# Performance work log

Hardware: AMD Instinct MI355X
Metric: run time of the kernel (lower is better)

The kernel has to match this reference:

```python
import jax, jax.numpy as jnp
import numpy as np

N_NODES = 100_000
N_EDGES = 1_600_000
N_GRAPHS = 1_000
VOCAB = 65
D_IN = 128
D_HID = 128


def setup_inputs() -> dict:
    key = jax.random.key(0)
    ks = jax.random.split(key, 12)
    x = jax.random.randint(ks[0], (N_NODES,), 0, VOCAB)
    edge_index = jax.random.randint(ks[1], (2, N_EDGES), 0, N_NODES)
    batch = jnp.sort(jax.random.randint(ks[2], (N_NODES,), 0, N_GRAPHS))

    def lin(k, fan_in, fan_out):
        bound = 1.0 / np.sqrt(fan_in)
        kw, kb = jax.random.split(k)
        W = jax.random.uniform(kw, (fan_in, fan_out), jnp.float32, -bound, bound)
        b = jax.random.uniform(kb, (fan_out,), jnp.float32, -bound, bound)
        return W, b

    emb = jax.random.normal(ks[3], (VOCAB, D_IN), jnp.float32)
    W1, b1 = lin(ks[4], D_IN, D_HID)
    W2, b2 = lin(ks[5], D_HID, D_HID)
    W3, b3 = lin(ks[6], D_HID, D_HID)
    Wf, bf = lin(ks[7], D_HID, 1)
    return {"x": x, "edge_index": edge_index, "batch": batch, "emb": emb,
            "W1": W1, "b1": b1, "W2": W2, "b2": b2, "W3": W3, "b3": b3,
            "Wf": Wf, "bf": bf}


def gcn_conv(h, W, b, src, dst, n):
    # PyG GCNConv: add self-loops, symmetric normalization D^-1/2 A_hat D^-1/2,
    # transform then aggregate messages at dst.
    h = h @ W                                             # [N, H]
    deg = jnp.zeros((n,), h.dtype).at[dst].add(1.0) + 1.0  # self-loop adds 1
    dinv = jax.lax.rsqrt(deg)                             # [N]
    coef = dinv[src] * dinv[dst]                          # [E]
    agg = jax.ops.segment_sum(h[src] * coef[:, None], dst, num_segments=n)
    return agg + h * (dinv * dinv)[:, None] + b           # self-loop term + bias


def reference(x, edge_index, batch, emb, W1, b1, W2, b2, W3, b3, Wf, bf):
    # Embedding with max_norm=1: renormalize looked-up rows to norm <= 1.
    e = emb[x]                                            # [N, D_IN]
    nrm = jnp.linalg.norm(e, axis=-1, keepdims=True)
    e = e * jnp.minimum(1.0, 1.0 / jnp.maximum(nrm, 1e-7))

    src, dst = edge_index[0], edge_index[1]
    h = jax.nn.relu(gcn_conv(e, W1, b1, src, dst, N_NODES))
    h = jax.nn.relu(gcn_conv(h, W2, b2, src, dst, N_NODES))
    h = jax.nn.relu(gcn_conv(h, W3, b3, src, dst, N_NODES))

    g = jax.ops.segment_max(h, batch, num_segments=N_GRAPHS)  # [G, H]
    return (g @ Wf + bf).ravel()                               # [G]
```

## Files before the change

kernel.cpp:

```cpp
#include <hip/hip_runtime.h>
#include <hip/hip_bf16.h>

#define N_NODES  100000
#define N_EDGES  1600000
#define N_GRAPHS 1000
#define D        128
#define CAP      64
#define NBKT     256
#define N_BUCKETS ((N_NODES + NBKT - 1) / NBKT)
#define HWGS     256
#define EPW      ((N_EDGES + HWGS - 1) / HWGS)
#define BNDB     ((N_NODES + 255) / 256)

typedef __attribute__((ext_vector_type(8))) short bf16x8;
typedef __attribute__((ext_vector_type(4))) float f32x4;

__device__ inline f32x4 mfma16(bf16x8 a, bf16x8 b, f32x4 c) {
    return __builtin_amdgcn_mfma_f32_16x16x32_bf16(a, b, c, 0, 0, 0);
}

__device__ inline unsigned short f2bf(float f) {
    unsigned u = __float_as_uint(f);
    unsigned r = u + 0x7fffu + ((u >> 16) & 1u);
    return (unsigned short)(r >> 16);
}

__global__ __launch_bounds__(256) void k_hist(const int* __restrict__ dst,
                                              int* __restrict__ bcnt,
                                              int* __restrict__ wgoff,
                                              const float* __restrict__ W1,
                                              const float* __restrict__ W2,
                                              const float* __restrict__ W3,
                                              short* __restrict__ frag,
                                              const int* __restrict__ batch,
                                              int* __restrict__ gstart,
                                              int* __restrict__ gend) {
    int w = blockIdx.x, t = threadIdx.x;
    if (w >= HWGS + 3) {
        int gid = (w - HWGS - 3) * 256 + t;
        if (gid < N_NODES) {
            int b = batch[gid];
            if (gid == 0 || batch[gid - 1] != b) gstart[b] = gid;
            if (gid == N_NODES - 1 || batch[gid + 1] != b) gend[b] = gid + 1;
        }
        return;
    }
    if (w >= HWGS) {
        int L = w - HWGS;
        const float* W = (L == 0) ? W1 : (L == 1) ? W2 : W3;
        short* fh = frag + (size_t)L * 16384;
        #pragma unroll
        for (int f = 0; f < 8; f++) {
            int id = t + f * 256;
            int lane = id & 63, kb = (id >> 6) & 3, nt = id >> 8;
            int k0 = kb * 32 + (lane >> 4) * 8;
            int n  = nt * 16 + (lane & 15);
            bf16x8 vh;
            #pragma unroll
            for (int j = 0; j < 8; j++)
                vh[j] = (short)f2bf(W[(k0 + j) * 128 + n]);
            *(bf16x8*)&fh[id * 8] = vh;
        }
        return;
    }
    __shared__ int hist[N_BUCKETS];
    for (int b = t; b < N_BUCKETS; b += 256) hist[b] = 0;
    __syncthreads();
    int e0 = w * EPW, e1 = min(e0 + EPW, N_EDGES);
    for (int i = e0 + t; i < e1; i += 256)
        atomicAdd(&hist[dst[i] >> 8], 1);
    __syncthreads();
    for (int b = t; b < N_BUCKETS; b += 256) {
        int h = hist[b];
        wgoff[w * N_BUCKETS + b] = h ? atomicAdd(&bcnt[b], h) : 0;
    }
}

__global__ __launch_bounds__(256) void k_scat(const int* __restrict__ src,
                                              const int* __restrict__ dst,
                                              const int* __restrict__ bcnt,
                                              const int* __restrict__ wgoff,
                                              int* __restrict__ ep) {
    __shared__ int sc[2][512];
    __shared__ int boff_s[N_BUCKETS];
    __shared__ int cnt[N_BUCKETS];
    int t = threadIdx.x, w = blockIdx.x;
    for (int i = t; i < 512; i += 256) sc[0][i] = (i < N_BUCKETS) ? bcnt[i] : 0;
    for (int b = t; b < N_BUCKETS; b += 256) cnt[b] = 0;
    __syncthreads();
    int pp = 0;
    for (int off = 1; off < 512; off <<= 1) {
        for (int i = t; i < 512; i += 256) {
            int v = sc[pp][i];
            if (i >= off) v += sc[pp][i - off];
            sc[1 - pp][i] = v;
        }
        __syncthreads();
        pp ^= 1;
    }
    for (int i = t; i < N_BUCKETS; i += 256) boff_s[i] = i ? sc[pp][i - 1] : 0;
    __syncthreads();
    int e0 = w * EPW, e1 = min(e0 + EPW, N_EDGES);
    for (int i = e0 + t; i < e1; i += 256) {
        int d = dst[i], b = d >> 8;
        int r = atomicAdd(&cnt[b], 1);
        ep[boff_s[b] + wgoff[w * N_BUCKETS + b] + r] = (src[i] << 8) | (d & 255);
    }
}

__global__ __launch_bounds__(256) void k_ell(const int* __restrict__ ep,
                                             const int* __restrict__ bcnt,
                                             int* __restrict__ ell,
                                             int* __restrict__ fill) {
    __shared__ int red[256];
    __shared__ int cnt_s[NBKT];
    __shared__ int ell_s[NBKT * CAP];
    int t = threadIdx.x, b = blockIdx.x;
    int partial = 0;
    for (int i = t; i < b; i += 256) partial += bcnt[i];
    red[t] = partial;
    for (int i = t; i < NBKT; i += 256) cnt_s[i] = 0;
    __syncthreads();
    for (int off = 128; off; off >>= 1) {
        if (t < off) red[t] += red[t + off];
        __syncthreads();
    }
    int e0 = red[0];
    int e1 = e0 + bcnt[b];
    int nb0 = b * NBKT;
    int nn = min(NBKT, N_NODES - nb0);
    for (int i = e0 + t; i < e1; i += 256) {
        int e = ep[i];
        int ln = e & 255;
        int r = atomicAdd(&cnt_s[ln], 1);
        if (r < CAP) ell_s[ln * CAP + r] = (int)((unsigned)e >> 8);
    }
    __syncthreads();
    for (int i = t; i < nn * CAP; i += 256)
        ell[(size_t)nb0 * CAP + i] = ell_s[i];
    if (t < nn) fill[nb0 + t] = cnt_s[t];
}

__device__ inline void gemm_body(const short* Bf,
                                 const bf16x8* a0, const bf16x8* a1,
                                 f32x4 acc[2][8], int lane) {
    #pragma unroll
    for (int kb = 0; kb < 4; kb++)
        #pragma unroll
        for (int nt = 0; nt < 8; nt++) {
            bf16x8 b = *(const bf16x8*)&Bf[((nt * 4 + kb) * 64 + lane) * 8];
            acc[0][nt] = mfma16(a0[kb], b, acc[0][nt]);
            acc[1][nt] = mfma16(a1[kb], b, acc[1][nt]);
        }
}

__device__ inline void gemm_epilogue(f32x4 acc[2][8], const int* fill,
                                     unsigned short* Cb, size_t r0,
                                     int quad, int col) {
    #pragma unroll
    for (int r = 0; r < 2; r++) {
        size_t row = r0 + r * 16 + quad * 4;
        #pragma unroll
        for (int g = 0; g < 4; g++) {
            float dv = (row + g < N_NODES)
                         ? 1.0f / sqrtf((float)fill[row + g] + 1.0f) : 0.f;
            #pragma unroll
            for (int nt = 0; nt < 8; nt++)
                Cb[(row + g) * D + nt * 16 + col] = f2bf(acc[r][nt][g] * dv);
        }
    }
}

__global__ __launch_bounds__(256) void k_gemm1e(const int* __restrict__ x,
                                                const float* __restrict__ emb,
                                                const short* __restrict__ frag,
                                                const int* __restrict__ fill,
                                                unsigned short* __restrict__ Cb) {
    __shared__ short Bfrag[16384];
    int t = threadIdx.x;
    {
        const int4* g4 = (const int4*)frag;
        int4* l4 = (int4*)Bfrag;
        #pragma unroll
        for (int i = 0; i < 8; i++) l4[t + i * 256] = g4[t + i * 256];
    }
    int w = t >> 6, lane = t & 63;
    int quad = lane >> 4, col = lane & 15;
    size_t r0 = (size_t)blockIdx.x * 128 + w * 32;

    bf16x8 a0[4], a1[4];
    {
        size_t ra = r0 + col, rb = r0 + 16 + col;
        int xa = (ra < N_NODES) ? x[ra] : 0;
        int xb = (rb < N_NODES) ? x[rb] : 0;
        float va[32], vb[32];
        float ssa = 0.f, ssb = 0.f;
        #pragma unroll
        for (int kb = 0; kb < 4; kb++) {
            float4 pa0 = *(const float4*)&emb[(size_t)xa * D + kb * 32 + quad * 8];
            float4 pa1 = *(const float4*)&emb[(size_t)xa * D + kb * 32 + quad * 8 + 4];
            float4 pb0 = *(const float4*)&emb[(size_t)xb * D + kb * 32 + quad * 8];
            float4 pb1 = *(const float4*)&emb[(size_t)xb * D + kb * 32 + quad * 8 + 4];
            va[kb*8+0]=pa0.x; va[kb*8+1]=pa0.y; va[kb*8+2]=pa0.z; va[kb*8+3]=pa0.w;
            va[kb*8+4]=pa1.x; va[kb*8+5]=pa1.y; va[kb*8+6]=pa1.z; va[kb*8+7]=pa1.w;
            vb[kb*8+0]=pb0.x; vb[kb*8+1]=pb0.y; vb[kb*8+2]=pb0.z; vb[kb*8+3]=pb0.w;
            vb[kb*8+4]=pb1.x; vb[kb*8+5]=pb1.y; vb[kb*8+6]=pb1.z; vb[kb*8+7]=pb1.w;
            #pragma unroll
            for (int j = 0; j < 8; j++) { ssa += va[kb*8+j]*va[kb*8+j];
                                          ssb += vb[kb*8+j]*vb[kb*8+j]; }
        }
        ssa += __shfl_xor(ssa, 16); ssa += __shfl_xor(ssa, 32);
        ssb += __shfl_xor(ssb, 16); ssb += __shfl_xor(ssb, 32);
        float sca = fminf(1.0f, 1.0f / fmaxf(sqrtf(ssa), 1e-7f));
        float scb = fminf(1.0f, 1.0f / fmaxf(sqrtf(ssb), 1e-7f));
        #pragma unroll
        for (int kb = 0; kb < 4; kb++) {
            bf16x8 fa, fb;
            #pragma unroll
            for (int j = 0; j < 8; j++) {
                fa[j] = (short)f2bf(va[kb*8+j] * sca);
                fb[j] = (short)f2bf(vb[kb*8+j] * scb);
            }
            a0[kb] = fa; a1[kb] = fb;
        }
    }
    f32x4 acc[2][8];
    #pragma unroll
    for (int r = 0; r < 2; r++)
        #pragma unroll
        for (int n = 0; n < 8; n++) acc[r][n] = (f32x4){0.f, 0.f, 0.f, 0.f};
    __syncthreads();
    gemm_body(Bfrag, a0, a1, acc, lane);
    gemm_epilogue(acc, fill, Cb, r0, quad, col);
}

__global__ __launch_bounds__(256) void k_gemm(const unsigned short* __restrict__ A,
                                              const short* __restrict__ frag,
                                              const int* __restrict__ fill,
                                              unsigned short* __restrict__ Cb) {
    __shared__ short Bfrag[16384];
    int t = threadIdx.x;
    {
        const int4* g4 = (const int4*)frag;
        int4* l4 = (int4*)Bfrag;
        #pragma unroll
        for (int i = 0; i < 8; i++) l4[t + i * 256] = g4[t + i * 256];
    }
    __syncthreads();
    int w = t >> 6, lane = t & 63;
    int quad = lane >> 4, col = lane & 15;
    size_t r0 = (size_t)blockIdx.x * 128 + w * 32;
    bf16x8 a0[4], a1[4];
    #pragma unroll
    for (int kb = 0; kb < 4; kb++) {
        a0[kb] = *(const bf16x8*)&A[(r0 + col)      * D + kb * 32 + quad * 8];
        a1[kb] = *(const bf16x8*)&A[(r0 + 16 + col) * D + kb * 32 + quad * 8];
    }
    f32x4 acc[2][8];
    #pragma unroll
    for (int r = 0; r < 2; r++)
        #pragma unroll
        for (int n = 0; n < 8; n++) acc[r][n] = (f32x4){0.f, 0.f, 0.f, 0.f};
    gemm_body(Bfrag, a0, a1, acc, lane);
    gemm_epilogue(acc, fill, Cb, r0, quad, col);
}

__device__ inline void acc8(float* acc, int4 r) {
    unsigned u0 = (unsigned)r.x, u1 = (unsigned)r.y,
             u2 = (unsigned)r.z, u3 = (unsigned)r.w;
    acc[0] += __uint_as_float(u0 << 16);
    acc[1] += __uint_as_float(u0 & 0xffff0000u);
    acc[2] += __uint_as_float(u1 << 16);
    acc[3] += __uint_as_float(u1 & 0xffff0000u);
    acc[4] += __uint_as_float(u2 << 16);
    acc[5] += __uint_as_float(u2 & 0xffff0000u);
    acc[6] += __uint_as_float(u3 << 16);
    acc[7] += __uint_as_float(u3 & 0xffff0000u);
}

#define LOADGRP(R, S, IT)                                                    \
    {                                                                        \
        _Pragma("unroll")                                                    \
        for (int k = 0; k < 4; k++) {                                        \
            int s = __shfl((S), (IT) * 16 + k * 4 + quad);                   \
            R[k] = *(const int4*)&hw2[((unsigned)s << 7) + cOff];            \
        }                                                                    \
    }
#define ACCGRP(A, R)                                                         \
    {                                                                        \
        _Pragma("unroll")                                                    \
        for (int k = 0; k < 4; k++) acc8((A), R[k]);                         \
    }

__global__ __launch_bounds__(256) void k_agg(const unsigned short* __restrict__ hw2,
                                             unsigned short* __restrict__ hout,
                                             const int* __restrict__ fill,
                                             const int* __restrict__ ell,
                                             const float* __restrict__ bias) {
    int w = threadIdx.x >> 6, lane = threadIdx.x & 63;
    int na = blockIdx.x * 8 + w * 2;
    int nb = na + 1;
    if (na >= N_NODES) return;
    int quad = lane >> 4;
    int l16  = lane & 15;
    unsigned cOff = (unsigned)(l16 << 3);

    int fa = __builtin_amdgcn_readfirstlane(fill[na]);
    int fb = __builtin_amdgcn_readfirstlane(fill[nb]);
    int ca = min(fa, CAP), cb = min(fb, CAP);
    int sa = (lane < ca) ? ell[na * CAP + lane] : N_NODES;
    int sb = (lane < cb) ? ell[nb * CAP + lane] : N_NODES;
    int ia = (ca + 15) >> 4; ia += (ia == 0);
    int ib = (cb + 15) >> 4; ib += (ib == 0);

    float accA[8], accB[8];
    #pragma unroll
    for (int c = 0; c < 8; c++) { accA[c] = 0.f; accB[c] = 0.f; }

    int4 A0[4], A1[4], B0[4], B1[4];
    LOADGRP(A0, sa, 0);
    LOADGRP(B0, sb, 0);
    if (1 < ia) LOADGRP(A1, sa, 1);
    ACCGRP(accA, A0);
    if (1 < ib) LOADGRP(B1, sb, 1);
    ACCGRP(accB, B0);
    if (ia > 1 || ib > 1) {
        if (2 < ia) LOADGRP(A0, sa, 2);
        if (1 < ia) ACCGRP(accA, A1);
        if (2 < ib) LOADGRP(B0, sb, 2);
        if (1 < ib) ACCGRP(accB, B1);
        if (ia > 2 || ib > 2) {
            if (3 < ia) LOADGRP(A1, sa, 3);
            if (2 < ia) ACCGRP(accA, A0);
            if (3 < ib) LOADGRP(B1, sb, 3);
            if (2 < ib) ACCGRP(accB, B0);
            if (3 < ia) ACCGRP(accA, A1);
            if (3 < ib) ACCGRP(accB, B1);
        }
    }

    #pragma unroll
    for (int c = 0; c < 8; c++) {
        accA[c] += __shfl_xor(accA[c], 16);
        accA[c] += __shfl_xor(accA[c], 32);
        accB[c] += __shfl_xor(accB[c], 16);
        accB[c] += __shfl_xor(accB[c], 32);
    }
    if (quad < 2) {
        int   n   = quad ? nb : na;
        int   fr  = quad ? fb : fa;
        float* acc = quad ? accB : accA;
        int4 sr = *(const int4*)&hw2[((unsigned)n << 7) + cOff];
        acc8(acc, sr);
        float di = 1.0f / sqrtf((float)fr + 1.0f);
        float4 bA = *(const float4*)&bias[l16 * 8];
        float4 bB = *(const float4*)&bias[l16 * 8 + 4];
        float o[8];
        o[0] = fmaxf(acc[0] * di + bA.x, 0.f);
        o[1] = fmaxf(acc[1] * di + bA.y, 0.f);
        o[2] = fmaxf(acc[2] * di + bA.z, 0.f);
        o[3] = fmaxf(acc[3] * di + bA.w, 0.f);
        o[4] = fmaxf(acc[4] * di + bB.x, 0.f);
        o[5] = fmaxf(acc[5] * di + bB.y, 0.f);
        o[6] = fmaxf(acc[6] * di + bB.z, 0.f);
        o[7] = fmaxf(acc[7] * di + bB.w, 0.f);
        int4 pk;
        pk.x = (int)((unsigned)f2bf(o[0]) | ((unsigned)f2bf(o[1]) << 16));
        pk.y = (int)((unsigned)f2bf(o[2]) | ((unsigned)f2bf(o[3]) << 16));
        pk.z = (int)((unsigned)f2bf(o[4]) | ((unsigned)f2bf(o[5]) << 16));
        pk.w = (int)((unsigned)f2bf(o[6]) | ((unsigned)f2bf(o[7]) << 16));
        *(int4*)&hout[((unsigned)n << 7) + cOff] = pk;
    }
}

__global__ __launch_bounds__(256) void k_pool(const unsigned short* __restrict__ h,
                                              const int* __restrict__ gstart,
                                              const int* __restrict__ gend,
                                              const float* __restrict__ Wf,
                                              const float* __restrict__ bf,
                                              float* __restrict__ out) {
    __shared__ float2 sm[4][64];
    int g = blockIdx.x;
    int w = threadIdx.x >> 6, lane = threadIdx.x & 63;
    int s = gstart[g], e = gend[g];
    float2 m = make_float2(-3.402823466e38f, -3.402823466e38f);
    for (int i = s + w; i < e; i += 4) {
        unsigned u = ((const unsigned*)(h + (size_t)i * D))[lane];
        m.x = fmaxf(m.x, __uint_as_float(u << 16));
        m.y = fmaxf(m.y, __uint_as_float(u & 0xffff0000u));
    }
    sm[w][lane] = m;
    __syncthreads();
    if (w == 0) {
        float2 a = sm[0][lane], b2 = sm[1][lane], c = sm[2][lane], d = sm[3][lane];
        m.x = fmaxf(fmaxf(a.x, b2.x), fmaxf(c.x, d.x));
        m.y = fmaxf(fmaxf(a.y, b2.y), fmaxf(c.y, d.y));
        float2 wf = ((const float2*)Wf)[lane];
        float val = m.x * wf.x + m.y * wf.y;
        #pragma unroll
        for (int off = 32; off; off >>= 1) val += __shfl_xor(val, off);
        if (lane == 0) out[g] = val + bf[0];
    }
}

extern "C" void kernel_launch(void* const* d_in, const int* in_sizes, int n_in,
                              void* d_out, int out_size, void* d_ws, size_t ws_size,
                              hipStream_t stream) {
    const int*   x    = (const int*)d_in[0];
    const int*   ei   = (const int*)d_in[1];
    const int*   batch= (const int*)d_in[2];
    const float* emb  = (const float*)d_in[3];
    const float* W1   = (const float*)d_in[4];
    const float* b1   = (const float*)d_in[5];
    const float* W2   = (const float*)d_in[6];
    const float* b2   = (const float*)d_in[7];
    const float* W3   = (const float*)d_in[8];
    const float* b3   = (const float*)d_in[9];
    const float* Wf   = (const float*)d_in[10];
    const float* bf   = (const float*)d_in[11];
    float* out = (float*)d_out;

    const int* src = ei;
    const int* dst = ei + N_EDGES;

    char* p = (char*)d_ws;
    unsigned short* hAb  = (unsigned short*)p; p += (size_t)(N_NODES + 128) * D * 2;
    unsigned short* hwb  = (unsigned short*)p; p += (size_t)(N_NODES + 128) * D * 2;
    int*            ep   = (int*)hwb;
    int*   fill     = (int*)p;              p += (size_t)N_NODES * 4;
    int*   gbounds  = (int*)p;              p += (size_t)2 * N_GRAPHS * 4;
    int*   ell      = (int*)p;              p += (size_t)N_NODES * CAP * 4;
    int*   wgoff    = (int*)p;              p += (size_t)HWGS * N_BUCKETS * 4;
    int*   bcnt     = (int*)p;              p += (size_t)(N_BUCKETS + 4) * 4;
    short* wfrag    = (short*)p;            p += (size_t)3 * 16384 * 2;
    (void)p;
    int* gstart = gbounds;
    int* gend   = gbounds + N_GRAPHS;

    hipMemsetAsync(bcnt, 0, (size_t)N_BUCKETS * 4, stream);

    const int GB = (N_NODES + 127) / 128;
    const int AB = N_NODES / 8;

    k_hist<<<HWGS + 3 + BNDB, 256, 0, stream>>>(dst, bcnt, wgoff, W1, W2, W3,
                                                wfrag, batch, gstart, gend);
    k_scat<<<HWGS, 256, 0, stream>>>(src, dst, bcnt, wgoff, ep);
    k_ell <<<N_BUCKETS, 256, 0, stream>>>(ep, bcnt, ell, fill);

    k_gemm1e<<<GB, 256, 0, stream>>>(x, emb, wfrag, fill, hwb);
    k_agg   <<<AB, 256, 0, stream>>>(hwb, hAb, fill, ell, b1);
    k_gemm<<<GB, 256, 0, stream>>>(hAb, wfrag + 16384, fill, hwb);
    k_agg <<<AB, 256, 0, stream>>>(hwb, hAb, fill, ell, b2);
    k_gemm<<<GB, 256, 0, stream>>>(hAb, wfrag + 32768, fill, hwb);
    k_agg <<<AB, 256, 0, stream>>>(hwb, hAb, fill, ell, b3);

    k_pool<<<N_GRAPHS, 256, 0, stream>>>(hAb, gstart, gend, Wf, bf, out);
}
```

Measured before the change: 374.5 us.

## Replace histogram-prefix edge bucketing with fixed-slot per-workgroup scatter

Drops the separate histogram kernel, the global bucket-count memset and the prefix scan. Each workgroup now scatters its edges straight into a fixed 64-slot region per (bucket, workgroup) and records per-segment counts. The ELL builder walks these padded segments instead of a compacted edge array. This removes a launch and a global synchronisation point, but the ELL kernel reads more sparsely populated memory, and edges are silently dropped if any workgroup gives a bucket more than 64 edges.

```diff
diff --git a/kernel.cpp b/kernel.cpp
--- a/kernel.cpp
+++ b/kernel.cpp
@@ -11,6 +11,7 @@
 #define HWGS     256
 #define EPW      ((N_EDGES + HWGS - 1) / HWGS)
 #define BNDB     ((N_NODES + 255) / 256)
+#define SLOT     64
 
 typedef __attribute__((ext_vector_type(8))) short bf16x8;
 typedef __attribute__((ext_vector_type(4))) float f32x4;
@@ -25,9 +26,10 @@
     return (unsigned short)(r >> 16);
 }
 
-__global__ __launch_bounds__(256) void k_hist(const int* __restrict__ dst,
-                                              int* __restrict__ bcnt,
-                                              int* __restrict__ wgoff,
+__global__ __launch_bounds__(256) void k_scat(const int* __restrict__ src,
+                                              const int* __restrict__ dst,
+                                              int* __restrict__ ep2,
+                                              int* __restrict__ cnt,
                                               const float* __restrict__ W1,
                                               const float* __restrict__ W2,
                                               const float* __restrict__ W3,
@@ -63,79 +65,46 @@
         }
         return;
     }
-    __shared__ int hist[N_BUCKETS];
-    for (int b = t; b < N_BUCKETS; b += 256) hist[b] = 0;
-    __syncthreads();
-    int e0 = w * EPW, e1 = min(e0 + EPW, N_EDGES);
-    for (int i = e0 + t; i < e1; i += 256)
-        atomicAdd(&hist[dst[i] >> 8], 1);
-    __syncthreads();
-    for (int b = t; b < N_BUCKETS; b += 256) {
-        int h = hist[b];
-        wgoff[w * N_BUCKETS + b] = h ? atomicAdd(&bcnt[b], h) : 0;
-    }
-}
-
-__global__ __launch_bounds__(256) void k_scat(const int* __restrict__ src,
-                                              const int* __restrict__ dst,
-                                              const int* __restrict__ bcnt,
-                                              const int* __restrict__ wgoff,
-                                              int* __restrict__ ep) {
-    __shared__ int sc[2][512];
-    __shared__ int boff_s[N_BUCKETS];
-    __shared__ int cnt[N_BUCKETS];
-    int t = threadIdx.x, w = blockIdx.x;
-    for (int i = t; i < 512; i += 256) sc[0][i] = (i < N_BUCKETS) ? bcnt[i] : 0;
-    for (int b = t; b < N_BUCKETS; b += 256) cnt[b] = 0;
-    __syncthreads();
-    int pp = 0;
-    for (int off = 1; off < 512; off <<= 1) {
-        for (int i = t; i < 512; i += 256) {
-            int v = sc[pp][i];
-            if (i >= off) v += sc[pp][i - off];
-            sc[1 - pp][i] = v;
-        }
-        __syncthreads();
-        pp ^= 1;
-    }
-    for (int i = t; i < N_BUCKETS; i += 256) boff_s[i] = i ? sc[pp][i - 1] : 0;
+    __shared__ int cnt_l[N_BUCKETS];
+    for (int b = t; b < N_BUCKETS; b += 256) cnt_l[b] = 0;
     __syncthreads();
     int e0 = w * EPW, e1 = min(e0 + EPW, N_EDGES);
     for (int i = e0 + t; i < e1; i += 256) {
         int d = dst[i], b = d >> 8;
-        int r = atomicAdd(&cnt[b], 1);
-        ep[boff_s[b] + wgoff[w * N_BUCKETS + b] + r] = (src[i] << 8) | (d & 255);
-    }
-}
-
-__global__ __launch_bounds__(256) void k_ell(const int* __restrict__ ep,
-                                             const int* __restrict__ bcnt,
+        int r = atomicAdd(&cnt_l[b], 1);
+        if (r < SLOT)
+            ep2[(size_t)b * (HWGS * SLOT) + w * SLOT + r] =
+                (src[i] << 8) | (d & 255);
+    }
+    __syncthreads();
+    for (int b = t; b < N_BUCKETS; b += 256)
+        cnt[w * N_BUCKETS + b] = cnt_l[b];
+}
+
+__global__ __launch_bounds__(256) void k_ell(const int* __restrict__ ep2,
+                                             const int* __restrict__ cnt,
                                              int* __restrict__ ell,
                                              int* __restrict__ fill) {
-    __shared__ int red[256];
+    __shared__ int cseg[HWGS];
     __shared__ int cnt_s[NBKT];
     __shared__ int ell_s[NBKT * CAP];
     int t = threadIdx.x, b = blockIdx.x;
-    int partial = 0;
-    for (int i = t; i < b; i += 256) partial += bcnt[i];
-    red[t] = partial;
+    cseg[t] = min(cnt[t * N_BUCKETS + b], SLOT);
     for (int i = t; i < NBKT; i += 256) cnt_s[i] = 0;
     __syncthreads();
-    for (int off = 128; off; off >>= 1) {
-        if (t < off) red[t] += red[t + off];
-        __syncthreads();
-    }
-    int e0 = red[0];
-    int e1 = e0 + bcnt[b];
+    size_t base = (size_t)b * (HWGS * SLOT);
+    for (int i = t; i < HWGS * SLOT; i += 256) {
+        int w = i >> 6, slot = i & (SLOT - 1);
+        if (slot < cseg[w]) {
+            int e = ep2[base + i];
+            int ln = e & 255;
+            int r = atomicAdd(&cnt_s[ln], 1);
+            if (r < CAP) ell_s[ln * CAP + r] = (int)((unsigned)e >> 8);
+        }
+    }
+    __syncthreads();
     int nb0 = b * NBKT;
     int nn = min(NBKT, N_NODES - nb0);
-    for (int i = e0 + t; i < e1; i += 256) {
-        int e = ep[i];
-        int ln = e & 255;
-        int r = atomicAdd(&cnt_s[ln], 1);
-        if (r < CAP) ell_s[ln * CAP + r] = (int)((unsigned)e >> 8);
-    }
-    __syncthreads();
     for (int i = t; i < nn * CAP; i += 256)
         ell[(size_t)nb0 * CAP + i] = ell_s[i];
     if (t < nn) fill[nb0 + t] = cnt_s[t];
@@ -426,26 +395,22 @@
     char* p = (char*)d_ws;
     unsigned short* hAb  = (unsigned short*)p; p += (size_t)(N_NODES + 128) * D * 2;
     unsigned short* hwb  = (unsigned short*)p; p += (size_t)(N_NODES + 128) * D * 2;
-    int*            ep   = (int*)hwb;
+    int*            ep2  = (int*)hwb;
     int*   fill     = (int*)p;              p += (size_t)N_NODES * 4;
     int*   gbounds  = (int*)p;              p += (size_t)2 * N_GRAPHS * 4;
     int*   ell      = (int*)p;              p += (size_t)N_NODES * CAP * 4;
-    int*   wgoff    = (int*)p;              p += (size_t)HWGS * N_BUCKETS * 4;
-    int*   bcnt     = (int*)p;              p += (size_t)(N_BUCKETS + 4) * 4;
+    int*   cnt      = (int*)p;              p += (size_t)HWGS * N_BUCKETS * 4;
     short* wfrag    = (short*)p;            p += (size_t)3 * 16384 * 2;
     (void)p;
     int* gstart = gbounds;
     int* gend   = gbounds + N_GRAPHS;
 
-    hipMemsetAsync(bcnt, 0, (size_t)N_BUCKETS * 4, stream);
-
     const int GB = (N_NODES + 127) / 128;
     const int AB = N_NODES / 8;
 
-    k_hist<<<HWGS + 3 + BNDB, 256, 0, stream>>>(dst, bcnt, wgoff, W1, W2, W3,
+    k_scat<<<HWGS + 3 + BNDB, 256, 0, stream>>>(src, dst, ep2, cnt, W1, W2, W3,
                                                 wfrag, batch, gstart, gend);
-    k_scat<<<HWGS, 256, 0, stream>>>(src, dst, bcnt, wgoff, ep);
-    k_ell <<<N_BUCKETS, 256, 0, stream>>>(ep, bcnt, ell, fill);
+    k_ell <<<N_BUCKETS, 256, 0, stream>>>(ep2, cnt, ell, fill);
 
     k_gemm1e<<<GB, 256, 0, stream>>>(x, emb, wfrag, fill, hwb);
     k_agg   <<<AB, 256, 0, stream>>>(hwb, hAb, fill, ell, b1);
```

New measurement: 380.7 us. Within noise of the previous version (+1.7%).
